# Performance work log

Measured on AMD Instinct MI355X. Metric: run time of the kernel, lower is better.

Reference implementation:

```python
import jax, jax.numpy as jnp
import numpy as np

H = 1024  # hidden_features
I = 64    # input_dims
O = 2     # output_dims
T = 4096  # timesteps


def setup_inputs() -> dict:
    key = jax.random.key(0)
    ks = jax.random.split(key, 12)
    s = 1.0 / np.sqrt(H)  # torch LSTMCell/Linear init scale
    return {
        "x_in":  jax.random.normal(ks[0], (T, I), dtype=jnp.float32),
        "W_ih1": jax.random.uniform(ks[1], (4 * H, I), jnp.float32, -s, s),
        "W_hh1": jax.random.uniform(ks[2], (4 * H, H), jnp.float32, -s, s),
        "b_ih1": jax.random.uniform(ks[3], (4 * H,), jnp.float32, -s, s),
        "b_hh1": jax.random.uniform(ks[4], (4 * H,), jnp.float32, -s, s),
        "W_ih2": jax.random.uniform(ks[5], (4 * H, H), jnp.float32, -s, s),
        "W_hh2": jax.random.uniform(ks[6], (4 * H, H), jnp.float32, -s, s),
        "b_ih2": jax.random.uniform(ks[7], (4 * H,), jnp.float32, -s, s),
        "b_hh2": jax.random.uniform(ks[8], (4 * H,), jnp.float32, -s, s),
        "W_out": jax.random.uniform(ks[9], (O, H), jnp.float32, -s, s),
        "b_out": jax.random.uniform(ks[10], (O,), jnp.float32, -s, s),
    }


def _lstm_cell(x, h, c, W_ih, W_hh, b_ih, b_hh):
    # PyTorch LSTMCell gate order: i, f, g, o
    gates = x @ W_ih.T + b_ih + h @ W_hh.T + b_hh  # [4H]
    i, f, g, o = jnp.split(gates, 4)
    i = jax.nn.sigmoid(i)
    f = jax.nn.sigmoid(f)
    g = jnp.tanh(g)
    o = jax.nn.sigmoid(o)
    c_new = f * c + i * g
    h_new = o * jnp.tanh(c_new)
    return h_new, c_new


def reference(x_in, W_ih1, W_hh1, b_ih1, b_hh1,
              W_ih2, W_hh2, b_ih2, b_hh2, W_out, b_out):
    def step(carry, x_t):
        h1, c1, h2, c2 = carry
        h1, c1 = _lstm_cell(x_t, h1, c1, W_ih1, W_hh1, b_ih1, b_hh1)
        h2, c2 = _lstm_cell(h1, h2, c2, W_ih2, W_hh2, b_ih2, b_hh2)
        out = h2 @ W_out.T + b_out  # [O]
        return (h1, c1, h2, c2), out

    z = jnp.zeros((H,), dtype=x_in.dtype)
    init = (z, z, z, z)
    _, outputs = jax.lax.scan(step, init, x_in)  # outputs: [T, O]
    return outputs
```

## Files before the change

### kernel.cpp

```cpp
#include <hip/hip_runtime.h>
#include <math.h>


#define HID 1024
#define DIN 64
#define TSTEPS 4096
#define NWG 256
#define TPB 512

typedef unsigned long long u64;
typedef unsigned int u32;
typedef _Float16 f16x2 __attribute__((ext_vector_type(2)));
typedef __fp16   g16x2 __attribute__((ext_vector_type(2)));

#define H2_OFF 2048
#define WS_NEED_U64 (2048ull + 4097ull * 1024ull)
#define WS_NEED_BYTES (WS_NEED_U64 * 8ull)
#define WS_ZERO_BYTES 32768

#define WLDS_U4 (8 * 512)
#define H1S_OFF (WLDS_U4 * 16)
#define H2S_OFF (H1S_OFF + 640 * 4)
#define DYN_LDS_BYTES (H2S_OFF + 640 * 4)

__device__ __forceinline__ float sigmoid_f(float v) {
    return 1.0f / (1.0f + __expf(-v));
}
__device__ __forceinline__ float tanh_f(float v) {
    return 2.0f / (1.0f + __expf(-2.0f * v)) - 1.0f;
}

__device__ __forceinline__ void st_pair(u64* p, float h, u32 tag) {
    u64 pk = ((u64)tag << 32) | (u64)__float_as_uint(h);
    __hip_atomic_store(p, pk, __ATOMIC_RELAXED, __HIP_MEMORY_SCOPE_AGENT);
}
__device__ __forceinline__ u64 ld_pair(const u64* p) {
    return __hip_atomic_load(p, __ATOMIC_RELAXED, __HIP_MEMORY_SCOPE_AGENT);
}
#define PTAG(v) ((u32)((v) >> 32))
#define PVAL(v) (__uint_as_float((u32)(v)))

union U32H2 { u32 u; f16x2 h; g16x2 g; };

__device__ __forceinline__ u32 pk2(float a, float b) {
    U32H2 t; t.g = __builtin_amdgcn_cvt_pkrtz(a, b); return t.u;
}

#if defined(__has_builtin)
#if __has_builtin(__builtin_amdgcn_fdot2)
#define HAS_FDOT2 1
#endif
#endif

__device__ __forceinline__ float dot2f(u32 a, u32 b, float c) {
    U32H2 x, y; x.u = a; y.u = b;
#ifdef HAS_FDOT2
    return __builtin_amdgcn_fdot2(x.h, y.h, c, false);
#else
    float r = fmaf((float)x.h.x, (float)y.h.x, c);
    return fmaf((float)x.h.y, (float)y.h.y, r);
#endif
}

#define PIN_W1() asm volatile("" : "+v"(w1p0), "+v"(w1p1), "+v"(w1p2), \
    "+v"(w1p3), "+v"(w1p4), "+v"(w1p5), "+v"(w1p6), "+v"(w1p7), \
    "+v"(w1p8), "+v"(w1p9), "+v"(w1pA), "+v"(w1pB), \
    "+v"(w1pC), "+v"(w1pD), "+v"(w1pE), "+v"(w1pF))

#define ASTEP(j, P0, P1, P2, P3) do {                               \
    uint4 hv = *(const uint4*)(h1s + hbase + 4*(j));                \
    uint4 w2 = wlds[(j)*512 + tid];                                 \
    a0 = dot2f(hv.x, P0, a0); a1 = dot2f(hv.y, P1, a1);             \
    a0 = dot2f(hv.z, P2, a0); a1 = dot2f(hv.w, P3, a1);             \
    e0 = dot2f(hv.x, w2.x, e0); e1 = dot2f(hv.y, w2.y, e1);         \
    e0 = dot2f(hv.z, w2.z, e0); e1 = dot2f(hv.w, w2.w, e1);         \
} while (0)

#define BSTEP(j) do {                                               \
    uint4 gv = *(const uint4*)(h2s + hbase + 4*(j));                \
    uint4 w3 = wlds[(4+(j))*512 + tid];                             \
    e0 = dot2f(gv.x, w3.x, e0); e1 = dot2f(gv.y, w3.y, e1);         \
    e0 = dot2f(gv.z, w3.z, e0); e1 = dot2f(gv.w, w3.w, e1);         \
} while (0)

__global__ void
__attribute__((amdgpu_flat_work_group_size(TPB, TPB), amdgpu_waves_per_eu(2, 2)))
lstm_persistent(
    const float* __restrict__ x,
    const float* __restrict__ Wih1, const float* __restrict__ Whh1,
    const float* __restrict__ bih1, const float* __restrict__ bhh1,
    const float* __restrict__ Wih2, const float* __restrict__ Whh2,
    const float* __restrict__ bih2, const float* __restrict__ bhh2,
    const float* __restrict__ Wout, const float* __restrict__ bout,
    float* __restrict__ out, u64* __restrict__ ws, int use_hist)
{
    const int wg   = blockIdx.x;
    const int tid  = threadIdx.x;
    const int wave = tid >> 6;
    const int lane = tid & 63;
    const int gate = tid >> 7;
    const int rsub = (tid >> 5) & 3;
    const int c    = tid & 31;
    const int row  = gate * HID + (wg << 2) + rsub;
    const int kbase = c << 5;

    u64* h1t = ws;
    u64* h2t = ws + H2_OFF;

    extern __shared__ __align__(16) char smem[];
    uint4* wlds = (uint4*)smem;
    u32*   h1s  = (u32*)(smem + H1S_OFF);
    u32*   h2s  = (u32*)(smem + H2S_OFF);

    {
        const float4* q2 = (const float4*)(Wih2 + (size_t)row * HID + kbase);
        const float4* q3 = (const float4*)(Whh2 + (size_t)row * HID + kbase);
        #pragma unroll
        for (int j = 0; j < 4; ++j) {
            float4 qa = q2[2*j], qb = q2[2*j+1];
            wlds[j * 512 + tid] = make_uint4(pk2(qa.x, qa.y), pk2(qa.z, qa.w),
                                             pk2(qb.x, qb.y), pk2(qb.z, qb.w));
        }
        #pragma unroll
        for (int j = 0; j < 4; ++j) {
            float4 qa = q3[2*j], qb = q3[2*j+1];
            wlds[(4+j) * 512 + tid] = make_uint4(pk2(qa.x, qa.y), pk2(qa.z, qa.w),
                                                 pk2(qb.x, qb.y), pk2(qb.z, qb.w));
        }
    }

    const float4* p1 = (const float4*)(Whh1 + (size_t)row * HID + kbase);
    float4 f0 = p1[0], f1 = p1[1], f2 = p1[2], f3 = p1[3];
    float4 f4 = p1[4], f5 = p1[5], f6 = p1[6], f7 = p1[7];
    u32 w1p0 = pk2(f0.x, f0.y), w1p1 = pk2(f0.z, f0.w);
    u32 w1p2 = pk2(f1.x, f1.y), w1p3 = pk2(f1.z, f1.w);
    u32 w1p4 = pk2(f2.x, f2.y), w1p5 = pk2(f2.z, f2.w);
    u32 w1p6 = pk2(f3.x, f3.y), w1p7 = pk2(f3.z, f3.w);
    u32 w1p8 = pk2(f4.x, f4.y), w1p9 = pk2(f4.z, f4.w);
    u32 w1pA = pk2(f5.x, f5.y), w1pB = pk2(f5.z, f5.w);
    u32 w1pC = pk2(f6.x, f6.y), w1pD = pk2(f6.z, f6.w);
    u32 w1pE = pk2(f7.x, f7.y), w1pF = pk2(f7.z, f7.w);
    PIN_W1();

    const float2 wx = *(const float2*)(Wih1 + (size_t)row * DIN + (c << 1));
    const float bsum1 = bih1[row] + bhh1[row];
    const float bsum2 = bih2[row] + bhh2[row];

    __shared__ float g1[4][4], g2[4][4];
    __shared__ float c1s[4], c2s[4];
    __shared__ float red0[8], red1[8];
    if (tid < 4) { c1s[tid] = 0.0f; c2s[tid] = 0.0f; }

    const int sdst = 20 * (tid >> 4) + (tid & 15);
    const int hbase = 20 * c;

    __syncthreads();

    for (int p = 0; p <= TSTEPS; ++p) {
        const u64* h1p = h1t + (size_t)(p & 1) * 1024 + (tid << 1);
        const int h2row_c = (p > 0) ? (use_hist ? (p - 1) : ((p - 1) & 1)) : 0;
        const u64* h2p = h2t + (size_t)h2row_c * 1024 + (tid << 1);
        const u32 want1 = (u32)p;
        const u32 want2 = (p >= 2) ? (u32)p : 0u;

        const int tx = (p < TSTEPS) ? p : 0;
        const float2 xv = *(const float2*)(x + (size_t)tx * DIN + (c << 1));

        u64 v1a, v1b;
        {
            int guard = 0;
            for (;;) {
                v1a = ld_pair(h1p); v1b = ld_pair(h1p + 1);
                if ((PTAG(v1a) == want1) & (PTAG(v1b) == want1)) break;
                if (++guard > (1 << 17)) break;
            }
        }
        u64 v2a = ld_pair(h2p), v2b = ld_pair(h2p + 1);

        PIN_W1();

        h1s[sdst] = pk2(PVAL(v1a), PVAL(v1b));
        __syncthreads();

        float a0 = 0.f, a1 = 0.f, e0 = 0.f, e1 = 0.f;
        ASTEP(0, w1p0, w1p1, w1p2, w1p3);
        ASTEP(1, w1p4, w1p5, w1p6, w1p7);
        ASTEP(2, w1p8, w1p9, w1pA, w1pB);
        ASTEP(3, w1pC, w1pD, w1pE, w1pF);
        a0 = fmaf(wx.x, xv.x, a0);
        a1 = fmaf(wx.y, xv.y, a1);

        float accA = a0 + a1;
        accA += __shfl_xor(accA, 1);
        accA += __shfl_xor(accA, 2);
        accA += __shfl_xor(accA, 4);
        accA += __shfl_xor(accA, 8);
        accA += __shfl_xor(accA, 16);
        if (c == 0) {
            float vA = accA + bsum1;
            g1[gate][rsub] = (gate == 2) ? tanh_f(vA) : sigmoid_f(vA);
        }

        {
            int guard = 0;
            while (!((PTAG(v2a) == want2) & (PTAG(v2b) == want2))) {
                v2a = ld_pair(h2p); v2b = ld_pair(h2p + 1);
                if (++guard > (1 << 17)) break;
            }
        }
        float sb0 = PVAL(v2a), sb1 = PVAL(v2b);
        h2s[sdst] = pk2(sb0, sb1);
        __syncthreads();

        if (p < TSTEPS && tid < 4) {
            float iv = g1[0][tid], fv = g1[1][tid];
            float gv = g1[2][tid], ov = g1[3][tid];
            float cn = fv * c1s[tid] + iv * gv;
            c1s[tid] = cn;
            st_pair(h1t + (size_t)((p + 1) & 1) * 1024 + (wg << 2) + tid,
                    ov * tanh_f(cn), (u32)(p + 1));
        }

        BSTEP(0); BSTEP(1); BSTEP(2); BSTEP(3);

        float accB = e0 + e1;
        accB += __shfl_xor(accB, 1);
        accB += __shfl_xor(accB, 2);
        accB += __shfl_xor(accB, 4);
        accB += __shfl_xor(accB, 8);
        accB += __shfl_xor(accB, 16);
        if (c == 0) {
            float vB = accB + bsum2;
            g2[gate][rsub] = (gate == 2) ? tanh_f(vB) : sigmoid_f(vB);
        }
        __syncthreads();

        if (p >= 1 && tid >= 4 && tid < 8) {
            int u = tid - 4;
            float iv = g2[0][u], fv = g2[1][u];
            float gv = g2[2][u], ov = g2[3][u];
            float cn = fv * c2s[u] + iv * gv;
            c2s[u] = cn;
            const int wr = use_hist ? p : (p & 1);
            st_pair(h2t + (size_t)wr * 1024 + (wg << 2) + u,
                    ov * tanh_f(cn), (u32)(p + 1));
        }

        if (!use_hist && wg == 0 && p >= 2) {
            const float2 wo0 = *(const float2*)(Wout + (tid << 1));
            const float2 wo1 = *(const float2*)(Wout + HID + (tid << 1));
            float q0 = wo0.x * sb0 + wo0.y * sb1;
            float q1 = wo1.x * sb0 + wo1.y * sb1;
            #pragma unroll
            for (int m = 1; m < 64; m <<= 1) {
                q0 += __shfl_xor(q0, m);
                q1 += __shfl_xor(q1, m);
            }
            if (lane == 0) { red0[wave] = q0; red1[wave] = q1; }
            __syncthreads();
            if (tid == 0) {
                float o0 = bout[0], o1 = bout[1];
                #pragma unroll
                for (int w = 0; w < 8; ++w) { o0 += red0[w]; o1 += red1[w]; }
                out[2*(p-2)+0] = o0;
                out[2*(p-2)+1] = o1;
            }
            __syncthreads();
        }
    }

    if (use_hist) {
        const float2 wo0 = *(const float2*)(Wout + (tid << 1));
        const float2 wo1 = *(const float2*)(Wout + HID + (tid << 1));
        const float bo0 = bout[0], bo1 = bout[1];
        for (int i = 0; i < 16; ++i) {
            const int t = (wg << 4) + i;
            const u64* hp = h2t + (size_t)(t + 1) * 1024 + (tid << 1);
            const u32 want = (u32)(t + 2);
            u64 va, vb; int guard = 0;
            for (;;) {
                va = ld_pair(hp); vb = ld_pair(hp + 1);
                if ((PTAG(va) == want) && (PTAG(vb) == want)) break;
                if (++guard > (1 << 15)) break;
            }
            float h0 = PVAL(va), h1v = PVAL(vb);
            float q0 = wo0.x * h0 + wo0.y * h1v;
            float q1 = wo1.x * h0 + wo1.y * h1v;
            #pragma unroll
            for (int m = 1; m < 64; m <<= 1) {
                q0 += __shfl_xor(q0, m);
                q1 += __shfl_xor(q1, m);
            }
            if (lane == 0) { red0[wave] = q0; red1[wave] = q1; }
            __syncthreads();
            if (tid == 0) {
                float o0 = bo0, o1 = bo1;
                #pragma unroll
                for (int w = 0; w < 8; ++w) { o0 += red0[w]; o1 += red1[w]; }
                out[2*t+0] = o0;
                out[2*t+1] = o1;
            }
            __syncthreads();
        }
    } else if (wg == 0) {
        const float2 wo0 = *(const float2*)(Wout + (tid << 1));
        const float2 wo1 = *(const float2*)(Wout + HID + (tid << 1));
        const u64* hp = h2t + (size_t)(TSTEPS & 1) * 1024 + (tid << 1);
        const u32 want = (u32)(TSTEPS + 1);
        u64 va, vb; int guard = 0;
        for (;;) {
            va = ld_pair(hp); vb = ld_pair(hp + 1);
            if ((PTAG(va) == want) && (PTAG(vb) == want)) break;
            if (++guard > (1 << 15)) break;
        }
        float h0 = PVAL(va), h1v = PVAL(vb);
        float q0 = wo0.x * h0 + wo0.y * h1v;
        float q1 = wo1.x * h0 + wo1.y * h1v;
        #pragma unroll
        for (int m = 1; m < 64; m <<= 1) {
            q0 += __shfl_xor(q0, m);
            q1 += __shfl_xor(q1, m);
        }
        if (lane == 0) { red0[wave] = q0; red1[wave] = q1; }
        __syncthreads();
        if (tid == 0) {
            float o0 = bout[0], o1 = bout[1];
            #pragma unroll
            for (int w = 0; w < 8; ++w) { o0 += red0[w]; o1 += red1[w]; }
            out[2*(TSTEPS-1)+0] = o0;
            out[2*(TSTEPS-1)+1] = o1;
        }
    }
}

extern "C" void kernel_launch(void* const* d_in, const int* in_sizes, int n_in,
                              void* d_out, int out_size, void* d_ws, size_t ws_size,
                              hipStream_t stream)
{
    const float* x    = (const float*)d_in[0];
    const float* Wih1 = (const float*)d_in[1];
    const float* Whh1 = (const float*)d_in[2];
    const float* bih1 = (const float*)d_in[3];
    const float* bhh1 = (const float*)d_in[4];
    const float* Wih2 = (const float*)d_in[5];
    const float* Whh2 = (const float*)d_in[6];
    const float* bih2 = (const float*)d_in[7];
    const float* bhh2 = (const float*)d_in[8];
    const float* Wout = (const float*)d_in[9];
    const float* bout = (const float*)d_in[10];
    float* out = (float*)d_out;
    u64*   ws  = (u64*)d_ws;

    const int use_hist = (ws_size >= WS_NEED_BYTES) ? 1 : 0;

    (void)hipFuncSetAttribute((const void*)lstm_persistent,
                              hipFuncAttributeMaxDynamicSharedMemorySize,
                              DYN_LDS_BYTES);

    (void)hipMemsetAsync(d_ws, 0, WS_ZERO_BYTES, stream);

    hipLaunchKernelGGL(lstm_persistent, dim3(NWG), dim3(TPB), DYN_LDS_BYTES,
                       stream,
                       x, Wih1, Whh1, bih1, bhh1,
                       Wih2, Whh2, bih2, bhh2,
                       Wout, bout, out, ws, use_hist);
}
```

Before: 7.560 ms.

## Split layer-1 and layer-2 work across wave groups with one barrier per step

Reassigns the 8 waves so waves 0-3 compute layer 1 (weights held in registers) and waves 4-7 compute layer 2 (weights in LDS), each thread covering all four gates of a row with shuffles that combine gates and cell state in registers rather than shared arrays. Double-buffered LDS hidden vectors cut the per-step barriers from three or four to one, and the output projection is folded into the layer-2 load path with a one-step delayed write. The aim is to shorten the serial per-timestep critical path. The cost is less parallelism per layer's dot product (twice the work per thread) and reindexed history buffers.

```diff
diff --git a/kernel.cpp b/kernel.cpp
--- a/kernel.cpp
+++ b/kernel.cpp
@@ -18,10 +18,14 @@
 #define WS_NEED_BYTES (WS_NEED_U64 * 8ull)
 #define WS_ZERO_BYTES 32768
 
-#define WLDS_U4 (8 * 512)
+#define WLDS_U4 4096
+#define HSTRIDE 36
+#define HBUF (HSTRIDE * 16)
 #define H1S_OFF (WLDS_U4 * 16)
-#define H2S_OFF (H1S_OFF + 640 * 4)
-#define DYN_LDS_BYTES (H2S_OFF + 640 * 4)
+#define H2S_OFF (H1S_OFF + 2 * HBUF * 4)
+#define DYN_LDS_BYTES (H2S_OFF + 2 * HBUF * 4)
+
+#define SADDR(s) (HSTRIDE * ((s) >> 5) + ((s) & 31))
 
 __device__ __forceinline__ float sigmoid_f(float v) {
     return 1.0f / (1.0f + __expf(-v));
@@ -41,7 +45,6 @@
 #define PVAL(v) (__uint_as_float((u32)(v)))
 
 union U32H2 { u32 u; f16x2 h; g16x2 g; };
-
 __device__ __forceinline__ u32 pk2(float a, float b) {
     U32H2 t; t.g = __builtin_amdgcn_cvt_pkrtz(a, b); return t.u;
 }
@@ -51,7 +54,6 @@
 #define HAS_FDOT2 1
 #endif
 #endif
-
 __device__ __forceinline__ float dot2f(u32 a, u32 b, float c) {
     U32H2 x, y; x.u = a; y.u = b;
 #ifdef HAS_FDOT2
@@ -62,23 +64,36 @@
 #endif
 }
 
-#define PIN_W1() asm volatile("" : "+v"(w1p0), "+v"(w1p1), "+v"(w1p2), \
-    "+v"(w1p3), "+v"(w1p4), "+v"(w1p5), "+v"(w1p6), "+v"(w1p7), \
-    "+v"(w1p8), "+v"(w1p9), "+v"(w1pA), "+v"(w1pB), \
-    "+v"(w1pC), "+v"(w1pD), "+v"(w1pE), "+v"(w1pF))
-
-#define ASTEP(j, P0, P1, P2, P3) do {                               \
-    uint4 hv = *(const uint4*)(h1s + hbase + 4*(j));                \
-    uint4 w2 = wlds[(j)*512 + tid];                                 \
-    a0 = dot2f(hv.x, P0, a0); a1 = dot2f(hv.y, P1, a1);             \
-    a0 = dot2f(hv.z, P2, a0); a1 = dot2f(hv.w, P3, a1);             \
+__device__ __forceinline__ uint4 pack4(float4 a, float4 b) {
+    return make_uint4(pk2(a.x, a.y), pk2(a.z, a.w),
+                      pk2(b.x, b.y), pk2(b.z, b.w));
+}
+
+#define PIN8() asm volatile("" : "+v"(qw0.x), "+v"(qw0.y), "+v"(qw0.z), \
+    "+v"(qw0.w), "+v"(qw1.x), "+v"(qw1.y), "+v"(qw1.z), "+v"(qw1.w),    \
+    "+v"(qw2.x), "+v"(qw2.y), "+v"(qw2.z), "+v"(qw2.w),                 \
+    "+v"(qw3.x), "+v"(qw3.y), "+v"(qw3.z), "+v"(qw3.w));                \
+    asm volatile("" : "+v"(qw4.x), "+v"(qw4.y), "+v"(qw4.z),            \
+    "+v"(qw4.w), "+v"(qw5.x), "+v"(qw5.y), "+v"(qw5.z), "+v"(qw5.w),    \
+    "+v"(qw6.x), "+v"(qw6.y), "+v"(qw6.z), "+v"(qw6.w),                 \
+    "+v"(qw7.x), "+v"(qw7.y), "+v"(qw7.z), "+v"(qw7.w))
+
+#define L1STEP(j, QW) do {                                          \
+    uint4 hv = *(const uint4*)(hbA + 4*(j));                        \
+    a0 = dot2f(hv.x, QW.x, a0); a1 = dot2f(hv.y, QW.y, a1);         \
+    a0 = dot2f(hv.z, QW.z, a0); a1 = dot2f(hv.w, QW.w, a1);         \
+} while (0)
+
+#define L2STEPA(j) do {                                             \
+    uint4 hv = *(const uint4*)(hbA + 4*(j));                        \
+    uint4 w2 = wlds[(j)*256 + k];                                   \
     e0 = dot2f(hv.x, w2.x, e0); e1 = dot2f(hv.y, w2.y, e1);         \
     e0 = dot2f(hv.z, w2.z, e0); e1 = dot2f(hv.w, w2.w, e1);         \
 } while (0)
 
-#define BSTEP(j) do {                                               \
-    uint4 gv = *(const uint4*)(h2s + hbase + 4*(j));                \
-    uint4 w3 = wlds[(4+(j))*512 + tid];                             \
+#define L2STEPB(j) do {                                             \
+    uint4 gv = *(const uint4*)(hbB + 4*(j));                        \
+    uint4 w3 = wlds[2048 + (j)*256 + k];                            \
     e0 = dot2f(gv.x, w3.x, e0); e1 = dot2f(gv.y, w3.y, e1);         \
     e0 = dot2f(gv.z, w3.z, e0); e1 = dot2f(gv.w, w3.w, e1);         \
 } while (0)
@@ -98,11 +113,12 @@
     const int tid  = threadIdx.x;
     const int wave = tid >> 6;
     const int lane = tid & 63;
-    const int gate = tid >> 7;
-    const int rsub = (tid >> 5) & 3;
-    const int c    = tid & 31;
-    const int row  = gate * HID + (wg << 2) + rsub;
-    const int kbase = c << 5;
+    const int isL2 = wave >> 2;
+    const int u    = wave & 3;
+    const int g    = lane & 3;
+    const int c    = lane >> 2;
+    const int k    = tid & 255;
+    const int R    = g * HID + (wg << 2) + u;
 
     u64* h1t = ws;
     u64* h2t = ws + H2_OFF;
@@ -112,170 +128,185 @@
     u32*   h1s  = (u32*)(smem + H1S_OFF);
     u32*   h2s  = (u32*)(smem + H2S_OFF);
 
-    {
-        const float4* q2 = (const float4*)(Wih2 + (size_t)row * HID + kbase);
-        const float4* q3 = (const float4*)(Whh2 + (size_t)row * HID + kbase);
+    __shared__ float red0[8], red1[8];
+    __shared__ float redF0[2][4], redF1[2][4];
+
+    uint4 qw0 = {0,0,0,0}, qw1 = {0,0,0,0}, qw2 = {0,0,0,0}, qw3 = {0,0,0,0};
+    uint4 qw4 = {0,0,0,0}, qw5 = {0,0,0,0}, qw6 = {0,0,0,0}, qw7 = {0,0,0,0};
+    float4 wx4 = make_float4(0.f, 0.f, 0.f, 0.f);
+    float4 wo0 = make_float4(0.f, 0.f, 0.f, 0.f);
+    float4 wo1 = make_float4(0.f, 0.f, 0.f, 0.f);
+    float bsum = 0.f;
+    float creg = 0.f;
+
+    if (!isL2) {
+        const float4* p1 = (const float4*)(Whh1 + (size_t)R * HID + (c << 6));
+        qw0 = pack4(p1[0],  p1[1]);
+        qw1 = pack4(p1[2],  p1[3]);
+        qw2 = pack4(p1[4],  p1[5]);
+        qw3 = pack4(p1[6],  p1[7]);
+        qw4 = pack4(p1[8],  p1[9]);
+        qw5 = pack4(p1[10], p1[11]);
+        qw6 = pack4(p1[12], p1[13]);
+        qw7 = pack4(p1[14], p1[15]);
+        wx4 = *(const float4*)(Wih1 + (size_t)R * DIN + (c << 2));
+        bsum = bih1[R] + bhh1[R];
+    } else {
+        const float4* q2 = (const float4*)(Wih2 + (size_t)R * HID + (c << 6));
+        const float4* q3 = (const float4*)(Whh2 + (size_t)R * HID + (c << 6));
         #pragma unroll
-        for (int j = 0; j < 4; ++j) {
-            float4 qa = q2[2*j], qb = q2[2*j+1];
-            wlds[j * 512 + tid] = make_uint4(pk2(qa.x, qa.y), pk2(qa.z, qa.w),
-                                             pk2(qb.x, qb.y), pk2(qb.z, qb.w));
-        }
+        for (int j = 0; j < 8; ++j)
+            wlds[j * 256 + k] = pack4(q2[2*j], q2[2*j+1]);
         #pragma unroll
-        for (int j = 0; j < 4; ++j) {
-            float4 qa = q3[2*j], qb = q3[2*j+1];
-            wlds[(4+j) * 512 + tid] = make_uint4(pk2(qa.x, qa.y), pk2(qa.z, qa.w),
-                                                 pk2(qb.x, qb.y), pk2(qb.z, qb.w));
+        for (int j = 0; j < 8; ++j)
+            wlds[2048 + j * 256 + k] = pack4(q3[2*j], q3[2*j+1]);
+        bsum = bih2[R] + bhh2[R];
+        if (!use_hist && wg == 0) {
+            wo0 = *(const float4*)(Wout + (k << 2));
+            wo1 = *(const float4*)(Wout + HID + (k << 2));
         }
     }
-
-    const float4* p1 = (const float4*)(Whh1 + (size_t)row * HID + kbase);
-    float4 f0 = p1[0], f1 = p1[1], f2 = p1[2], f3 = p1[3];
-    float4 f4 = p1[4], f5 = p1[5], f6 = p1[6], f7 = p1[7];
-    u32 w1p0 = pk2(f0.x, f0.y), w1p1 = pk2(f0.z, f0.w);
-    u32 w1p2 = pk2(f1.x, f1.y), w1p3 = pk2(f1.z, f1.w);
-    u32 w1p4 = pk2(f2.x, f2.y), w1p5 = pk2(f2.z, f2.w);
-    u32 w1p6 = pk2(f3.x, f3.y), w1p7 = pk2(f3.z, f3.w);
-    u32 w1p8 = pk2(f4.x, f4.y), w1p9 = pk2(f4.z, f4.w);
-    u32 w1pA = pk2(f5.x, f5.y), w1pB = pk2(f5.z, f5.w);
-    u32 w1pC = pk2(f6.x, f6.y), w1pD = pk2(f6.z, f6.w);
-    u32 w1pE = pk2(f7.x, f7.y), w1pF = pk2(f7.z, f7.w);
-    PIN_W1();
-
-    const float2 wx = *(const float2*)(Wih1 + (size_t)row * DIN + (c << 1));
-    const float bsum1 = bih1[row] + bhh1[row];
-    const float bsum2 = bih2[row] + bhh2[row];
-
-    __shared__ float g1[4][4], g2[4][4];
-    __shared__ float c1s[4], c2s[4];
-    __shared__ float red0[8], red1[8];
-    if (tid < 4) { c1s[tid] = 0.0f; c2s[tid] = 0.0f; }
-
-    const int sdst = 20 * (tid >> 4) + (tid & 15);
-    const int hbase = 20 * c;
+    PIN8();
 
     __syncthreads();
 
     for (int p = 0; p <= TSTEPS; ++p) {
-        const u64* h1p = h1t + (size_t)(p & 1) * 1024 + (tid << 1);
-        const int h2row_c = (p > 0) ? (use_hist ? (p - 1) : ((p - 1) & 1)) : 0;
-        const u64* h2p = h2t + (size_t)h2row_c * 1024 + (tid << 1);
-        const u32 want1 = (u32)p;
-        const u32 want2 = (p >= 2) ? (u32)p : 0u;
-
-        const int tx = (p < TSTEPS) ? p : 0;
-        const float2 xv = *(const float2*)(x + (size_t)tx * DIN + (c << 1));
-
-        u64 v1a, v1b;
-        {
+        const int buf = p & 1;
+
+        if (!isL2) {
+            const u64* hp = h1t + (size_t)buf * 1024 + (k << 2);
+            const u32 want = (u32)p;
+            u64 e0 = ld_pair(hp),     e1 = ld_pair(hp + 1);
+            u64 e2 = ld_pair(hp + 2), e3 = ld_pair(hp + 3);
             int guard = 0;
-            for (;;) {
-                v1a = ld_pair(h1p); v1b = ld_pair(h1p + 1);
-                if ((PTAG(v1a) == want1) & (PTAG(v1b) == want1)) break;
+            while ((PTAG(e0) != want) | (PTAG(e1) != want) |
+                   (PTAG(e2) != want) | (PTAG(e3) != want)) {
+                if (PTAG(e0) != want) e0 = ld_pair(hp);
+                if (PTAG(e1) != want) e1 = ld_pair(hp + 1);
+                if (PTAG(e2) != want) e2 = ld_pair(hp + 2);
+                if (PTAG(e3) != want) e3 = ld_pair(hp + 3);
                 if (++guard > (1 << 17)) break;
             }
-        }
-        u64 v2a = ld_pair(h2p), v2b = ld_pair(h2p + 1);
-
-        PIN_W1();
-
-        h1s[sdst] = pk2(PVAL(v1a), PVAL(v1b));
+            u32* hb = h1s + buf * HBUF;
+            hb[SADDR(2*k)]     = pk2(PVAL(e0), PVAL(e1));
+            hb[SADDR(2*k + 1)] = pk2(PVAL(e2), PVAL(e3));
+        } else {
+            float v0 = 0.f, v1 = 0.f, v2 = 0.f, v3 = 0.f;
+            if (p >= 1) {
+                const u32 want = (p >= 2) ? (u32)p : 0u;
+                const int row2 = (p >= 2) ? (use_hist ? (p - 2) : (p & 1)) : 1;
+                const u64* hp = h2t + (size_t)row2 * 1024 + (k << 2);
+                u64 e0 = ld_pair(hp),     e1 = ld_pair(hp + 1);
+                u64 e2 = ld_pair(hp + 2), e3 = ld_pair(hp + 3);
+                int guard = 0;
+                while ((PTAG(e0) != want) | (PTAG(e1) != want) |
+                       (PTAG(e2) != want) | (PTAG(e3) != want)) {
+                    if (PTAG(e0) != want) e0 = ld_pair(hp);
+                    if (PTAG(e1) != want) e1 = ld_pair(hp + 1);
+                    if (PTAG(e2) != want) e2 = ld_pair(hp + 2);
+                    if (PTAG(e3) != want) e3 = ld_pair(hp + 3);
+                    if (++guard > (1 << 17)) break;
+                }
+                v0 = PVAL(e0); v1 = PVAL(e1); v2 = PVAL(e2); v3 = PVAL(e3);
+            }
+            u32* hb = h2s + buf * HBUF;
+            hb[SADDR(2*k)]     = pk2(v0, v1);
+            hb[SADDR(2*k + 1)] = pk2(v2, v3);
+
+            if (!use_hist && wg == 0 && p >= 2) {
+                float q0 = wo0.x*v0 + wo0.y*v1 + wo0.z*v2 + wo0.w*v3;
+                float q1 = wo1.x*v0 + wo1.y*v1 + wo1.z*v2 + wo1.w*v3;
+                #pragma unroll
+                for (int m = 1; m < 64; m <<= 1) {
+                    q0 += __shfl_xor(q0, m);
+                    q1 += __shfl_xor(q1, m);
+                }
+                if (lane == 0) { redF0[buf][u] = q0; redF1[buf][u] = q1; }
+            }
+        }
+
         __syncthreads();
 
-        float a0 = 0.f, a1 = 0.f, e0 = 0.f, e1 = 0.f;
-        ASTEP(0, w1p0, w1p1, w1p2, w1p3);
-        ASTEP(1, w1p4, w1p5, w1p6, w1p7);
-        ASTEP(2, w1p8, w1p9, w1pA, w1pB);
-        ASTEP(3, w1pC, w1pD, w1pE, w1pF);
-        a0 = fmaf(wx.x, xv.x, a0);
-        a1 = fmaf(wx.y, xv.y, a1);
-
-        float accA = a0 + a1;
-        accA += __shfl_xor(accA, 1);
-        accA += __shfl_xor(accA, 2);
-        accA += __shfl_xor(accA, 4);
-        accA += __shfl_xor(accA, 8);
-        accA += __shfl_xor(accA, 16);
-        if (c == 0) {
-            float vA = accA + bsum1;
-            g1[gate][rsub] = (gate == 2) ? tanh_f(vA) : sigmoid_f(vA);
-        }
-
-        {
-            int guard = 0;
-            while (!((PTAG(v2a) == want2) & (PTAG(v2b) == want2))) {
-                v2a = ld_pair(h2p); v2b = ld_pair(h2p + 1);
-                if (++guard > (1 << 17)) break;
-            }
-        }
-        float sb0 = PVAL(v2a), sb1 = PVAL(v2b);
-        h2s[sdst] = pk2(sb0, sb1);
-        __syncthreads();
-
-        if (p < TSTEPS && tid < 4) {
-            float iv = g1[0][tid], fv = g1[1][tid];
-            float gv = g1[2][tid], ov = g1[3][tid];
-            float cn = fv * c1s[tid] + iv * gv;
-            c1s[tid] = cn;
-            st_pair(h1t + (size_t)((p + 1) & 1) * 1024 + (wg << 2) + tid,
-                    ov * tanh_f(cn), (u32)(p + 1));
-        }
-
-        BSTEP(0); BSTEP(1); BSTEP(2); BSTEP(3);
-
-        float accB = e0 + e1;
-        accB += __shfl_xor(accB, 1);
-        accB += __shfl_xor(accB, 2);
-        accB += __shfl_xor(accB, 4);
-        accB += __shfl_xor(accB, 8);
-        accB += __shfl_xor(accB, 16);
-        if (c == 0) {
-            float vB = accB + bsum2;
-            g2[gate][rsub] = (gate == 2) ? tanh_f(vB) : sigmoid_f(vB);
-        }
-        __syncthreads();
-
-        if (p >= 1 && tid >= 4 && tid < 8) {
-            int u = tid - 4;
-            float iv = g2[0][u], fv = g2[1][u];
-            float gv = g2[2][u], ov = g2[3][u];
-            float cn = fv * c2s[u] + iv * gv;
-            c2s[u] = cn;
-            const int wr = use_hist ? p : (p & 1);
-            st_pair(h2t + (size_t)wr * 1024 + (wg << 2) + u,
-                    ov * tanh_f(cn), (u32)(p + 1));
-        }
-
-        if (!use_hist && wg == 0 && p >= 2) {
-            const float2 wo0 = *(const float2*)(Wout + (tid << 1));
-            const float2 wo1 = *(const float2*)(Wout + HID + (tid << 1));
-            float q0 = wo0.x * sb0 + wo0.y * sb1;
-            float q1 = wo1.x * sb0 + wo1.y * sb1;
-            #pragma unroll
-            for (int m = 1; m < 64; m <<= 1) {
-                q0 += __shfl_xor(q0, m);
-                q1 += __shfl_xor(q1, m);
-            }
-            if (lane == 0) { red0[wave] = q0; red1[wave] = q1; }
-            __syncthreads();
-            if (tid == 0) {
-                float o0 = bout[0], o1 = bout[1];
-                #pragma unroll
-                for (int w = 0; w < 8; ++w) { o0 += red0[w]; o1 += red1[w]; }
-                out[2*(p-2)+0] = o0;
-                out[2*(p-2)+1] = o1;
-            }
-            __syncthreads();
+        if (!isL2) {
+            if (p < TSTEPS) {
+                const u32* hbA = h1s + buf * HBUF + HSTRIDE * c;
+                float a0 = 0.f, a1 = 0.f;
+                L1STEP(0, qw0); L1STEP(1, qw1); L1STEP(2, qw2); L1STEP(3, qw3);
+                L1STEP(4, qw4); L1STEP(5, qw5); L1STEP(6, qw6); L1STEP(7, qw7);
+                const float4 xv4 = *(const float4*)(x + (size_t)p * DIN + (c << 2));
+                a0 = fmaf(wx4.x, xv4.x, a0); a1 = fmaf(wx4.y, xv4.y, a1);
+                a0 = fmaf(wx4.z, xv4.z, a0); a1 = fmaf(wx4.w, xv4.w, a1);
+                float acc = a0 + a1;
+                acc += __shfl_xor(acc, 4);
+                acc += __shfl_xor(acc, 8);
+                acc += __shfl_xor(acc, 16);
+                acc += __shfl_xor(acc, 32);
+                float val = acc + bsum;
+                val = (g == 2) ? tanh_f(val) : sigmoid_f(val);
+                float t1v = __shfl_xor(val, 1);
+                float t2v = __shfl_xor(val, 2);
+                float t3v = __shfl_xor(t1v, 2);
+                if (g == 0) {
+                    float cn = t1v * creg + val * t2v;
+                    creg = cn;
+                    float hh = t3v * tanh_f(cn);
+                    if (c == 0)
+                        st_pair(h1t + (size_t)((p + 1) & 1) * 1024 + (wg << 2) + u,
+                                hh, (u32)(p + 1));
+                }
+            }
+            PIN8();
+        } else {
+            if (!use_hist && wg == 0 && k == 0 && p >= 3) {
+                const int rb = (p - 1) & 1;
+                float o0 = bout[0] + redF0[rb][0] + redF0[rb][1]
+                                   + redF0[rb][2] + redF0[rb][3];
+                float o1 = bout[1] + redF1[rb][0] + redF1[rb][1]
+                                   + redF1[rb][2] + redF1[rb][3];
+                out[2*(p-3)+0] = o0;
+                out[2*(p-3)+1] = o1;
+            }
+            if (p >= 1) {
+                const u32* hbA = h1s + buf * HBUF + HSTRIDE * c;
+                const u32* hbB = h2s + buf * HBUF + HSTRIDE * c;
+                float e0 = 0.f, e1 = 0.f;
+                L2STEPA(0); L2STEPA(1); L2STEPA(2); L2STEPA(3);
+                L2STEPA(4); L2STEPA(5); L2STEPA(6); L2STEPA(7);
+                L2STEPB(0); L2STEPB(1); L2STEPB(2); L2STEPB(3);
+                L2STEPB(4); L2STEPB(5); L2STEPB(6); L2STEPB(7);
+                float acc = e0 + e1;
+                acc += __shfl_xor(acc, 4);
+                acc += __shfl_xor(acc, 8);
+                acc += __shfl_xor(acc, 16);
+                acc += __shfl_xor(acc, 32);
+                float val = acc + bsum;
+                val = (g == 2) ? tanh_f(val) : sigmoid_f(val);
+                float t1v = __shfl_xor(val, 1);
+                float t2v = __shfl_xor(val, 2);
+                float t3v = __shfl_xor(t1v, 2);
+                if (g == 0) {
+                    float cn = t1v * creg + val * t2v;
+                    creg = cn;
+                    float hh = t3v * tanh_f(cn);
+                    if (c == 0) {
+                        const int wr = use_hist ? (p - 1) : ((p - 1) & 1);
+                        st_pair(h2t + (size_t)wr * 1024 + (wg << 2) + u,
+                                hh, (u32)(p + 1));
+                    }
+                }
+            }
         }
     }
 
+    __syncthreads();
+
     if (use_hist) {
-        const float2 wo0 = *(const float2*)(Wout + (tid << 1));
-        const float2 wo1 = *(const float2*)(Wout + HID + (tid << 1));
+        const float2 wo0e = *(const float2*)(Wout + (tid << 1));
+        const float2 wo1e = *(const float2*)(Wout + HID + (tid << 1));
         const float bo0 = bout[0], bo1 = bout[1];
         for (int i = 0; i < 16; ++i) {
             const int t = (wg << 4) + i;
-            const u64* hp = h2t + (size_t)(t + 1) * 1024 + (tid << 1);
+            const u64* hp = h2t + (size_t)t * 1024 + (tid << 1);
             const u32 want = (u32)(t + 2);
             u64 va, vb; int guard = 0;
             for (;;) {
@@ -284,8 +315,8 @@
                 if (++guard > (1 << 15)) break;
             }
             float h0 = PVAL(va), h1v = PVAL(vb);
-            float q0 = wo0.x * h0 + wo0.y * h1v;
-            float q1 = wo1.x * h0 + wo1.y * h1v;
+            float q0 = wo0e.x * h0 + wo0e.y * h1v;
+            float q1 = wo1e.x * h0 + wo1e.y * h1v;
             #pragma unroll
             for (int m = 1; m < 64; m <<= 1) {
                 q0 += __shfl_xor(q0, m);
@@ -303,9 +334,17 @@
             __syncthreads();
         }
     } else if (wg == 0) {
-        const float2 wo0 = *(const float2*)(Wout + (tid << 1));
-        const float2 wo1 = *(const float2*)(Wout + HID + (tid << 1));
-        const u64* hp = h2t + (size_t)(TSTEPS & 1) * 1024 + (tid << 1);
+        if (tid == 256) {
+            float o0 = bout[0] + redF0[0][0] + redF0[0][1]
+                               + redF0[0][2] + redF0[0][3];
+            float o1 = bout[1] + redF1[0][0] + redF1[0][1]
+                               + redF1[0][2] + redF1[0][3];
+            out[2*(TSTEPS-2)+0] = o0;
+            out[2*(TSTEPS-2)+1] = o1;
+        }
+        const float2 wo0e = *(const float2*)(Wout + (tid << 1));
+        const float2 wo1e = *(const float2*)(Wout + HID + (tid << 1));
+        const u64* hp = h2t + (size_t)((TSTEPS - 1) & 1) * 1024 + (tid << 1);
         const u32 want = (u32)(TSTEPS + 1);
         u64 va, vb; int guard = 0;
         for (;;) {
@@ -314,8 +353,8 @@
             if (++guard > (1 << 15)) break;
         }
         float h0 = PVAL(va), h1v = PVAL(vb);
-        float q0 = wo0.x * h0 + wo0.y * h1v;
-        float q1 = wo1.x * h0 + wo1.y * h1v;
+        float q0 = wo0e.x * h0 + wo0e.y * h1v;
+        float q1 = wo1e.x * h0 + wo1e.y * h1v;
         #pragma unroll
         for (int m = 1; m < 64; m <<= 1) {
             q0 += __shfl_xor(q0, m);
```

After: 25.38 ms. 3.36x slower.
